# Kernel optimization log

Hardware: AMD Instinct MI355X
Metric: run time of the kernel (lower is better)

The kernel has to match this reference:

```python
import jax, jax.numpy as jnp
import numpy as np

B, S, D_MODEL, H, D_KV = 2, 2048, 1024, 16, 64
NUM_BUCKETS, MAX_DIST = 32, 128


def _relative_position_bucket(rel_pos, num_buckets=NUM_BUCKETS, max_distance=MAX_DIST):
    # bidirectional (encoder) bucketing, matching T5Attention._relative_position_bucket
    nb = num_buckets // 2
    buckets = (rel_pos > 0).astype(jnp.int32) * nb
    rel = jnp.abs(rel_pos)
    max_exact = nb // 2
    is_small = rel < max_exact
    rel_f = jnp.maximum(rel.astype(jnp.float32), 1.0)  # guard log(0); masked by is_small anyway
    large = max_exact + (
        jnp.log(rel_f / max_exact) / np.log(max_distance / max_exact) * (nb - max_exact)
    ).astype(jnp.int32)
    large = jnp.minimum(large, nb - 1)
    return buckets + jnp.where(is_small, rel, large)


def setup_inputs() -> dict:
    key = jax.random.key(0)
    ks = jax.random.split(key, 6)
    sc = 1.0 / np.sqrt(D_MODEL)
    return {
        "hidden_states": jax.random.normal(ks[0], (B, S, D_MODEL), jnp.float32),
        "Wq": jax.random.normal(ks[1], (D_MODEL, H * D_KV), jnp.float32) * sc,
        "Wk": jax.random.normal(ks[2], (D_MODEL, H * D_KV), jnp.float32) * sc,
        "Wv": jax.random.normal(ks[3], (D_MODEL, H * D_KV), jnp.float32) * sc,
        "Wo": jax.random.normal(ks[4], (H * D_KV, D_MODEL), jnp.float32) * sc,
        "rel_bias_table": jax.random.normal(ks[5], (NUM_BUCKETS, H), jnp.float32),
    }


def reference(hidden_states, Wq, Wk, Wv, Wo, rel_bias_table):
    b, s, _ = hidden_states.shape
    # projections (T5 uses no bias, scale=1.0 in attention)
    q = (hidden_states @ Wq).reshape(b, s, H, D_KV).transpose(0, 2, 1, 3)  # bhsd
    k = (hidden_states @ Wk).reshape(b, s, H, D_KV).transpose(0, 2, 1, 3)
    v = (hidden_states @ Wv).reshape(b, s, H, D_KV).transpose(0, 2, 1, 3)

    # relative position bias: [1, H, S, S]
    ctx = jnp.arange(s)[:, None]
    mem = jnp.arange(s)[None, :]
    buckets = _relative_position_bucket(mem - ctx)          # [S, S]
    pos_bias = rel_bias_table[buckets]                       # [S, S, H]
    pos_bias = pos_bias.transpose(2, 0, 1)[None]             # [1, H, S, S]

    scores = jnp.einsum("bhqd,bhkd->bhqk", q, k) + pos_bias  # scale = 1.0
    probs = jax.nn.softmax(scores, axis=-1)
    attn = jnp.einsum("bhqk,bhkd->bhqd", probs, v)
    attn = attn.transpose(0, 2, 1, 3).reshape(b, s, H * D_KV)
    return attn @ Wo
```

## Files before the change

kernel.cpp:

```cpp
#include <hip/hip_runtime.h>
#include <hip/hip_fp16.h>

#define S_LEN 2048
#define NH 16
#define DK 64
#define DM 1024
#define NB 2
#define QKV_SZ (NB * NH * S_LEN * DK)

typedef _Float16 half8 __attribute__((ext_vector_type(8)));
typedef _Float16 half4v __attribute__((ext_vector_type(4)));
typedef __fp16 fp16x2 __attribute__((ext_vector_type(2)));
typedef float f32x4 __attribute__((ext_vector_type(4)));

static __device__ __forceinline__ half4v pack4(const f32x4 v) {
  fp16x2 lo = __builtin_amdgcn_cvt_pkrtz(v[0], v[1]);
  fp16x2 hi = __builtin_amdgcn_cvt_pkrtz(v[2], v[3]);
  half4v r;
  ((fp16x2*)&r)[0] = lo;
  ((fp16x2*)&r)[1] = hi;
  return r;
}

#define GLL(gp, lp)                                                              \
  __builtin_amdgcn_global_load_lds(                                              \
      (const __attribute__((address_space(1))) unsigned int*)(gp),               \
      (__attribute__((address_space(3))) unsigned int*)(lp), 16, 0, 0)


__global__ __launch_bounds__(256) void conv_f32_f16(const float* __restrict__ in,
                                                    _Float16* __restrict__ out, int n4) {
  int i = blockIdx.x * 256 + threadIdx.x;
  if (i >= n4) return;
  float4 v = ((const float4*)in)[i];
  half4v o;
  o[0] = (_Float16)v.x; o[1] = (_Float16)v.y; o[2] = (_Float16)v.z; o[3] = (_Float16)v.w;
  ((half4v*)out)[i] = o;
}

__global__ __launch_bounds__(256) void transpose_conv4(
    const float* __restrict__ Wq, const float* __restrict__ Wk,
    const float* __restrict__ Wv, const float* __restrict__ Wo,
    _Float16* __restrict__ Wqkvt, _Float16* __restrict__ Wot) {
  __shared__ float tile[32][33];
  int z = blockIdx.z;
  const float* W = (z == 0) ? Wq : (z == 1) ? Wk : (z == 2) ? Wv : Wo;
  _Float16* Wt = (z < 3) ? (Wqkvt + (size_t)z * 1048576) : Wot;
  float scale = (z == 0) ? 1.44269504f : 1.0f;
  int tx = threadIdx.x, ty = threadIdx.y;
  int nx = blockIdx.x * 32 + tx;
  int ky = blockIdx.y * 32;
#pragma unroll
  for (int i = 0; i < 32; i += 8) tile[ty + i][tx] = W[(size_t)(ky + ty + i) * DM + nx];
  __syncthreads();
  int kx = ky + tx;
  int ny = blockIdx.x * 32;
#pragma unroll
  for (int i = 0; i < 32; i += 8)
    Wt[(size_t)(ny + ty + i) * DM + kx] = (_Float16)(tile[tx][ty + i] * scale);
}

__global__ __launch_bounds__(256) void bias_tab_kernel(const float* __restrict__ table,
                                                       float* __restrict__ tab) {
  int i = blockIdx.x * 256 + threadIdx.x;
  if (i >= NH * 4095) return;
  int h = i / 4095, r = i - h * 4095;
  int rel = r - 2047;
  int bucket = rel > 0 ? 16 : 0;
  int a = rel < 0 ? -rel : rel;
  if (a < 8) {
    bucket += a;
  } else {
    int lg = 31 - __clz(a * a);
    int large = 8 + (lg - 6);
    bucket += (large < 15 ? large : 15);
  }
  tab[i] = table[bucket * NH + h] * 1.44269504f;
}

template <int MODE>
__global__ __launch_bounds__(256) void gemm_f16(const _Float16* __restrict__ A,
                                                const _Float16* __restrict__ Bt,
                                                void* __restrict__ Cout,
                                                int M, int N, int K) {
  __shared__ _Float16 As[128 * 32];
  __shared__ _Float16 Bs[128 * 32];
  const int t = threadIdx.x;
  const int m0 = blockIdx.y * 128, n0 = blockIdx.x * 128;
  const int w = t >> 6, lane = t & 63, l15 = lane & 15, quad = lane >> 4;
  const int wr = (w >> 1) * 64, wc = (w & 1) * 64;
  const int swz = (quad ^ (l15 & 3)) * 8;

  f32x4 acc[4][4];
#pragma unroll
  for (int i = 0; i < 4; i++)
#pragma unroll
    for (int j = 0; j < 4; j++) acc[i][j] = (f32x4){0.f, 0.f, 0.f, 0.f};

  for (int k0 = 0; k0 < K; k0 += 32) {
    __syncthreads();
#pragma unroll
    for (int i = 0; i < 2; i++) {
      int id = t + 256 * i;
      int row = id >> 2, c = id & 3;
      int cg = c ^ (row & 3);
      GLL(A + (size_t)(m0 + row) * K + k0 + cg * 8, (char*)As + id * 16);
      GLL(Bt + (size_t)(n0 + row) * K + k0 + cg * 8, (char*)Bs + id * 16);
    }
    __syncthreads();
    half8 af[4], bf[4];
#pragma unroll
    for (int i = 0; i < 4; i++) af[i] = *(const half8*)(As + (wr + i * 16 + l15) * 32 + swz);
#pragma unroll
    for (int i = 0; i < 4; i++) bf[i] = *(const half8*)(Bs + (wc + i * 16 + l15) * 32 + swz);
#pragma unroll
    for (int i = 0; i < 4; i++)
#pragma unroll
      for (int j = 0; j < 4; j++)
        acc[i][j] = __builtin_amdgcn_mfma_f32_16x16x32_f16(af[i], bf[j], acc[i][j], 0, 0, 0);
  }

#pragma unroll
  for (int i = 0; i < 4; i++)
#pragma unroll
    for (int j = 0; j < 4; j++) {
      int row0 = m0 + wr + i * 16 + quad * 4;
      int col = n0 + wc + j * 16 + l15;
      if (MODE == 1) {
#pragma unroll
        for (int r = 0; r < 4; r++)
          ((float*)Cout)[(size_t)(row0 + r) * N + col] = acc[i][j][r];
      } else {
        int which = col >> 10, rem = col & 1023, hh = rem >> 6, dd = rem & 63;
        int bb = row0 >> 11, ss = row0 & 2047;
        _Float16* base = (_Float16*)Cout;
        if (which == 2) {
          *(half4v*)(base + (size_t)2 * QKV_SZ +
                     ((size_t)((bb * NH + hh) * DK + dd)) * S_LEN + ss) = pack4(acc[i][j]);
        } else {
#pragma unroll
          for (int r = 0; r < 4; r++)
            base[(size_t)which * QKV_SZ +
                 ((size_t)((bb * NH + hh) * S_LEN) + ss + r) * DK + dd] = (_Float16)acc[i][j][r];
        }
      }
    }
}

__global__ __launch_bounds__(256, 4) void attn_kernel(
    const _Float16* __restrict__ Q, const _Float16* __restrict__ K,
    const _Float16* __restrict__ Vt, const float* __restrict__ btab,
    _Float16* __restrict__ attn_out) {
  __shared__ _Float16 Ks[2][4096];
  __shared__ _Float16 Vs[2][4096];
  __shared__ float slab[512];

  const int t = threadIdx.x;
  const int Q0 = blockIdx.x * 64;
  const int h = blockIdx.y, b = blockIdx.z;
  const int w = t >> 6, lane = t & 63, l15 = lane & 15, quad = lane >> 4;
  const int qw0 = Q0 + w * 16;
  const int sw7 = l15 & 7;

  const _Float16* Qb = Q + (size_t)(b * NH + h) * S_LEN * DK;
  const _Float16* Kb = K + (size_t)(b * NH + h) * S_LEN * DK;
  const _Float16* Vb = Vt + (size_t)(b * NH + h) * S_LEN * DK;

  for (int i = t; i < 512; i += 256) slab[i] = btab[h * 4095 + 1791 + i];
  const float cbn = btab[h * 4095 + 1791 + 128];
  const float cbp = btab[h * 4095 + 1791 + 384];

  const int id0 = t, id1 = t + 256;
  const int r0_ = id0 >> 3, cg0 = (id0 & 7) ^ (r0_ & 7), p0 = r0_ & 31;
  const int sr0 = (r0_ & 32) | (((p0 >> 2) & 3) << 3) | ((p0 >> 4) << 2) | (p0 & 3);
  const int r1_ = id1 >> 3, cg1 = (id1 & 7) ^ (r1_ & 7), p1 = r1_ & 31;
  const int sr1 = (r1_ & 32) | (((p1 >> 2) & 3) << 3) | ((p1 >> 4) << 2) | (p1 & 3);
  const int kofa = sr0 * DK + cg0 * 8, kofb = sr1 * DK + cg1 * 8;
  const int vofa = r0_ * S_LEN + cg0 * 8, vofb = r1_ * S_LEN + cg1 * 8;
  const int lda = id0 * 16, ldb = id1 * 16;

#define STAGE(bs, kk0)                                   \
  do {                                                   \
    const _Float16* kp_ = Kb + (size_t)(kk0) * DK;       \
    const _Float16* vp_ = Vb + (kk0);                    \
    GLL(kp_ + kofa, (char*)Ks[bs] + lda);                \
    GLL(kp_ + kofb, (char*)Ks[bs] + ldb);                \
    GLL(vp_ + vofa, (char*)Vs[bs] + lda);                \
    GLL(vp_ + vofb, (char*)Vs[bs] + ldb);                \
  } while (0)

  half8 qf[2];
#pragma unroll
  for (int dh = 0; dh < 2; dh++)
    qf[dh] = *(const half8*)(Qb + (size_t)(qw0 + l15) * DK + dh * 32 + quad * 8);

  f32x4 o[4];
#pragma unroll
  for (int dt = 0; dt < 4; dt++) o[dt] = (f32x4){0.f, 0.f, 0.f, 0.f};
  f32x4 lac = (f32x4){0.f, 0.f, 0.f, 0.f};
  float m_ = -INFINITY;
  const half4v ones = {(_Float16)1.f, (_Float16)1.f, (_Float16)1.f, (_Float16)1.f};

  const int rd0 = l15 * 64 + (quad ^ sw7) * 8;
  const int rd1 = rd0 ^ 32;

  STAGE(0, 0);
  __syncthreads();

#define TILE(c, kk, stage_ok)                                                         \
  do {                                                                                \
    if (stage_ok) STAGE((c) ^ 1, (kk) + 64);   \
    const int dk0 = (kk) - qw0;                                                       \
    const bool farneg = (dk0 <= -191);                                                \
    const bool farpos = (dk0 >= 143);                                                 \
    const bool nearc = !(farneg || farpos);                                           \
    const float cb = farneg ? cbn : cbp;                                              \
    f32x4 st[4];                                                                      \
    if (nearc) {                                                                      \
      _Pragma("unroll") for (int kt = 0; kt < 4; kt++) {                              \
        int i0 = dk0 + (kt >> 1) * 32 + quad * 8 + (kt & 1) * 4 - l15 + 256;          \
        f32x4 v_;                                                                     \
        v_[0] = slab[i0]; v_[1] = slab[i0 + 1];                                       \
        v_[2] = slab[i0 + 2]; v_[3] = slab[i0 + 3];                                   \
        st[kt] = v_;                                                                  \
      }                                                                               \
    } else {                                                                          \
      _Pragma("unroll") for (int kt = 0; kt < 4; kt++)                                \
          st[kt] = (f32x4){0.f, 0.f, 0.f, 0.f};                                       \
    }                                                                                 \
    half8 kf0[4], kf1[4];                                                             \
    _Pragma("unroll") for (int kt = 0; kt < 4; kt++) {                                \
      kf0[kt] = *(const half8*)(&Ks[c][rd0 + kt * 1024]);                             \
      kf1[kt] = *(const half8*)(&Ks[c][rd1 + kt * 1024]);                             \
    }                                                                                 \
    __builtin_amdgcn_s_setprio(1);                                                    \
    _Pragma("unroll") for (int kt = 0; kt < 4; kt++) {                                \
      st[kt] = __builtin_amdgcn_mfma_f32_16x16x32_f16(kf0[kt], qf[0], st[kt], 0, 0, 0); \
      st[kt] = __builtin_amdgcn_mfma_f32_16x16x32_f16(kf1[kt], qf[1], st[kt], 0, 0, 0); \
    }                                                                                 \
    __builtin_amdgcn_s_setprio(0);                                                    \
                                                         \
    float x0 = fmaxf(fmaxf(st[0][0], st[0][1]), st[0][2]);                            \
    float x1 = fmaxf(fmaxf(st[0][3], st[1][0]), st[1][1]);                            \
    float x2 = fmaxf(fmaxf(st[1][2], st[1][3]), st[2][0]);                            \
    float x3 = fmaxf(fmaxf(st[2][1], st[2][2]), st[2][3]);                            \
    float x4 = fmaxf(fmaxf(st[3][0], st[3][1]), st[3][2]);                            \
    float cm = fmaxf(fmaxf(fmaxf(x0, x1), fmaxf(x2, x3)), fmaxf(x4, st[3][3]));       \
    cm = fmaxf(cm, __shfl_xor(cm, 16));                                               \
    cm = fmaxf(cm, __shfl_xor(cm, 32));                                               \
    float mc = nearc ? cm : cm + cb;                                                  \
    if (__any(mc > m_)) {           \
      float mnew = fmaxf(m_, mc);                                                     \
      float alpha = __builtin_amdgcn_exp2f(m_ - mnew);                                \
      m_ = mnew;                                                                      \
      lac *= alpha;                                                                   \
      _Pragma("unroll") for (int dt = 0; dt < 4; dt++) o[dt] *= alpha;                \
    }                                                                                 \
    float msub = nearc ? m_ : m_ - cb;                                                \
    half4v p16[4];                                                                    \
    _Pragma("unroll") for (int kt = 0; kt < 4; kt++) {                                \
      f32x4 p_;                                                                       \
      _Pragma("unroll") for (int r = 0; r < 4; r++)                                   \
          p_[r] = __builtin_amdgcn_exp2f(st[kt][r] - msub);                           \
      p16[kt] = pack4(p_);                                                            \
    }                                                                                 \
    __builtin_amdgcn_s_setprio(1);                                                    \
     \
    _Pragma("unroll") for (int kt = 0; kt < 4; kt++)                                  \
        lac = __builtin_amdgcn_mfma_f32_16x16x16f16(ones, p16[kt], lac, 0, 0, 0);     \
    _Pragma("unroll") for (int dt = 0; dt < 4; dt++) {                                \
      half8 va_ = *(const half8*)(&Vs[c][rd0 + dt * 1024]);                           \
      half8 vb_ = *(const half8*)(&Vs[c][rd1 + dt * 1024]);                           \
      half4v alo = {va_[0], va_[1], va_[2], va_[3]};                                  \
      half4v ahi = {va_[4], va_[5], va_[6], va_[7]};                                  \
      half4v blo = {vb_[0], vb_[1], vb_[2], vb_[3]};                                  \
      half4v bhi = {vb_[4], vb_[5], vb_[6], vb_[7]};                                  \
      o[dt] = __builtin_amdgcn_mfma_f32_16x16x16f16(alo, p16[0], o[dt], 0, 0, 0);     \
      o[dt] = __builtin_amdgcn_mfma_f32_16x16x16f16(ahi, p16[1], o[dt], 0, 0, 0);     \
      o[dt] = __builtin_amdgcn_mfma_f32_16x16x16f16(blo, p16[2], o[dt], 0, 0, 0);     \
      o[dt] = __builtin_amdgcn_mfma_f32_16x16x16f16(bhi, p16[3], o[dt], 0, 0, 0);     \
    }                                                                                 \
    __builtin_amdgcn_s_setprio(0);                                                    \
    __syncthreads();              \
  } while (0)

  for (int k0 = 0; k0 < S_LEN; k0 += 128) {
    TILE(0, k0, 1);
    TILE(1, k0 + 64, (k0 + 128 < S_LEN));
  }
#undef TILE
#undef STAGE

  float inv = 1.0f / lac[0];
  int q = qw0 + l15;
#pragma unroll
  for (int dt = 0; dt < 4; dt++) {
    f32x4 ov = o[dt] * inv;
    *(half4v*)(attn_out + ((size_t)(b * S_LEN + q)) * DM + h * DK + dt * 16 + quad * 4) =
        pack4(ov);
  }
}

extern "C" void kernel_launch(void* const* d_in, const int* in_sizes, int n_in,
                              void* d_out, int out_size, void* d_ws, size_t ws_size,
                              hipStream_t stream) {
  const float* hs  = (const float*)d_in[0];
  const float* Wq  = (const float*)d_in[1];
  const float* Wk  = (const float*)d_in[2];
  const float* Wv  = (const float*)d_in[3];
  const float* Wo  = (const float*)d_in[4];
  const float* tbl = (const float*)d_in[5];
  float* out = (float*)d_out;
  char* ws = (char*)d_ws;

  _Float16* Xh    = (_Float16*)(ws);
  _Float16* Wqkvt = (_Float16*)(ws + (8u << 20));
  _Float16* Wot   = (_Float16*)(ws + (14u << 20));
  _Float16* Qd    = (_Float16*)(ws + (16u << 20));
  _Float16* Kd    = Qd + (size_t)QKV_SZ;
  _Float16* Vd    = Qd + (size_t)2 * QKV_SZ;
  _Float16* Ah    = (_Float16*)(ws + (40u << 20));
  float*    btab  = (float*)(ws + (48u << 20));

  conv_f32_f16<<<4096, 256, 0, stream>>>(hs, Xh, (NB * S_LEN * DM) / 4);
  transpose_conv4<<<dim3(32, 32, 4), dim3(32, 8), 0, stream>>>(Wq, Wk, Wv, Wo, Wqkvt, Wot);
  bias_tab_kernel<<<256, 256, 0, stream>>>(tbl, btab);

  gemm_f16<0><<<dim3(24, 32), 256, 0, stream>>>(Xh, Wqkvt, (void*)Qd, NB * S_LEN, 3 * DM, DM);
  attn_kernel<<<dim3(S_LEN / 64, NH, NB), 256, 0, stream>>>(Qd, Kd, Vd, btab, Ah);
  gemm_f16<1><<<dim3(8, 32), 256, 0, stream>>>(Ah, Wot, (void*)out, NB * S_LEN, DM, DM);
}
```

Baseline: 215.7 us.

## Use narrower 128x64-tile GEMM for output projection and lazy softmax rescale

```diff
diff --git a/kernel.cpp b/kernel.cpp
--- a/kernel.cpp
+++ b/kernel.cpp
@@ -144,6 +144,63 @@
                  ((size_t)((bb * NH + hh) * S_LEN) + ss + r) * DK + dd] = (_Float16)acc[i][j][r];
         }
       }
+    }
+}
+
+__global__ __launch_bounds__(256) void gemm_f16_n64(const _Float16* __restrict__ A,
+                                                    const _Float16* __restrict__ Bt,
+                                                    float* __restrict__ C,
+                                                    int M, int N, int K) {
+  __shared__ _Float16 As[128 * 32];
+  __shared__ _Float16 Bs[64 * 32];
+  const int t = threadIdx.x;
+  const int m0 = blockIdx.y * 128, n0 = blockIdx.x * 64;
+  const int w = t >> 6, lane = t & 63, l15 = lane & 15, quad = lane >> 4;
+  const int wr = (w >> 1) * 64, wc = (w & 1) * 32;
+  const int swz = (quad ^ (l15 & 3)) * 8;
+
+  f32x4 acc[4][2];
+#pragma unroll
+  for (int i = 0; i < 4; i++)
+#pragma unroll
+    for (int j = 0; j < 2; j++) acc[i][j] = (f32x4){0.f, 0.f, 0.f, 0.f};
+
+  for (int k0 = 0; k0 < K; k0 += 32) {
+    __syncthreads();
+#pragma unroll
+    for (int i = 0; i < 2; i++) {
+      int id = t + 256 * i;
+      int row = id >> 2, c = id & 3;
+      int cg = c ^ (row & 3);
+      GLL(A + (size_t)(m0 + row) * K + k0 + cg * 8, (char*)As + id * 16);
+    }
+    {
+      int row = t >> 2, c = t & 3;
+      int cg = c ^ (row & 3);
+      GLL(Bt + (size_t)(n0 + row) * K + k0 + cg * 8, (char*)Bs + t * 16);
+    }
+    __syncthreads();
+    half8 af[4], bf[2];
+#pragma unroll
+    for (int i = 0; i < 4; i++) af[i] = *(const half8*)(As + (wr + i * 16 + l15) * 32 + swz);
+#pragma unroll
+    for (int j = 0; j < 2; j++) bf[j] = *(const half8*)(Bs + (wc + j * 16 + l15) * 32 + swz);
+#pragma unroll
+    for (int i = 0; i < 4; i++)
+#pragma unroll
+      for (int j = 0; j < 2; j++)
+        acc[i][j] = __builtin_amdgcn_mfma_f32_16x16x32_f16(af[i], bf[j], acc[i][j], 0, 0, 0);
+  }
+
+#pragma unroll
+  for (int i = 0; i < 4; i++)
+#pragma unroll
+    for (int j = 0; j < 2; j++) {
+      int row0 = m0 + wr + i * 16 + quad * 4;
+      int col = n0 + wc + j * 16 + l15;
+#pragma unroll
+      for (int r = 0; r < 4; r++)
+        C[(size_t)(row0 + r) * N + col] = acc[i][j][r];
     }
 }
 
@@ -249,7 +306,7 @@
     cm = fmaxf(cm, __shfl_xor(cm, 16));                                               \
     cm = fmaxf(cm, __shfl_xor(cm, 32));                                               \
     float mc = nearc ? cm : cm + cb;                                                  \
-    if (__any(mc > m_)) {           \
+    if (__any(mc > m_ + 8.f)) {     \
       float mnew = fmaxf(m_, mc);                                                     \
       float alpha = __builtin_amdgcn_exp2f(m_ - mnew);                                \
       m_ = mnew;                                                                      \
@@ -328,5 +385,5 @@
 
   gemm_f16<0><<<dim3(24, 32), 256, 0, stream>>>(Xh, Wqkvt, (void*)Qd, NB * S_LEN, 3 * DM, DM);
   attn_kernel<<<dim3(S_LEN / 64, NH, NB), 256, 0, stream>>>(Qd, Kd, Vd, btab, Ah);
-  gemm_f16<1><<<dim3(8, 32), 256, 0, stream>>>(Ah, Wot, (void*)out, NB * S_LEN, DM, DM);
-}
+  gemm_f16_n64<<<dim3(16, 32), 256, 0, stream>>>(Ah, Wot, out, NB * S_LEN, DM, DM);
+}
```

Result: faster. 210.4 us (-2.5%).
